# Performance work log

Measured on AMD Instinct MI355X. Metric: run time of the kernel, lower is better.

The kernel has to match this reference:

```python
import jax, jax.numpy as jnp
import numpy as np
from itertools import permutations as _permutations

N_ORB = 64
N_ALPHA = 5
N_BETA = 5
TEMP = 1.0
PERMS5 = jnp.asarray(np.array(list(_permutations(range(5))), dtype=np.int32))  # (120, 5)


def setup_inputs() -> dict:
    key = jax.random.key(0)
    ks = jax.random.split(key, 16)
    B = 8192
    s = 0.02
    inp = {
        "uniform_alpha": jax.random.uniform(ks[0], (B, N_ORB), dtype=jnp.float32),
        "uniform_beta": jax.random.uniform(ks[1], (B, N_ORB), dtype=jnp.float32),
        # learnable params
        "alpha_logits": jax.random.normal(ks[2], (N_ORB,), dtype=jnp.float32) * s,
        # alpha_to_beta: Linear(n_orb,128) -> SiLU -> Linear(128,64)
        "W1": jax.random.normal(ks[3], (N_ORB, 128), dtype=jnp.float32) * s,
        "b1": jnp.zeros((128,), jnp.float32),
        "W2": jax.random.normal(ks[4], (128, 64), dtype=jnp.float32) * s,
        "b2": jnp.zeros((64,), jnp.float32),
        # beta_conditioned_scorer: Linear(n_orb+64,256)->SiLU->Linear(256,256)->SiLU->Linear(256,n_orb)
        "V1": jax.random.normal(ks[5], (N_ORB + 64, 256), dtype=jnp.float32) * s,
        "c1": jnp.zeros((256,), jnp.float32),
        "V2": jax.random.normal(ks[6], (256, 256), dtype=jnp.float32) * s,
        "c2": jnp.zeros((256,), jnp.float32),
        "V3": jax.random.normal(ks[7], (256, N_ORB), dtype=jnp.float32) * s,
        "c3": jnp.zeros((N_ORB,), jnp.float32),
    }
    return inp


def _gumbel_topk(logits, uniform, k):
    """Straight-through Gumbel top-k mask. logits, uniform: (B, n)."""
    g = -jnp.log(-jnp.log(jnp.maximum(uniform, 1e-10)))
    perturbed = (logits + g) / TEMP
    _, top_idx = jax.lax.top_k(perturbed, k)                      # (B, k)
    B = logits.shape[0]
    one_hot = jnp.zeros_like(logits).at[jnp.arange(B)[:, None], top_idx].set(1.0)
    soft = jax.nn.softmax(perturbed, axis=-1)
    return one_hot - jax.lax.stop_gradient(soft) + soft


def _exact_pl_log_prob(logits, selection, k, perms):
    """log P(unordered top-k set) under Plackett-Luce, exact over k! orderings.

    logits: (B, n); selection: (B, n) soft/hard mask; perms: (P, k) static.
    """
    B, n = logits.shape
    P = perms.shape[0]
    _, sel_idx = jax.lax.top_k(selection, k)
    sel_idx = jnp.sort(sel_idx, axis=-1)                          # (B, k)
    perm_idx = sel_idx[:, perms]                                  # (B, P, k)
    lg = logits[:, None, :]                                       # (B, 1, n)
    remaining = jnp.ones((B, P, n), dtype=bool)
    lp = jnp.zeros((B, P), logits.dtype)
    bi = jnp.arange(B)[:, None]
    pi = jnp.arange(P)[None, :]
    for step in range(k):  # k is small and static (5)
        masked = jnp.where(remaining, lg, -jnp.inf)
        logp = jax.nn.log_softmax(masked, axis=-1)                # (B, P, n)
        idx = perm_idx[:, :, step]                                # (B, P)
        lp = lp + jnp.take_along_axis(logp, idx[..., None], axis=-1)[..., 0]
        remaining = remaining.at[bi, pi, idx].set(False)
    return jax.scipy.special.logsumexp(lp, axis=-1)              # (B,)


def reference(uniform_alpha, uniform_beta, alpha_logits, W1, b1, W2, b2,
              V1, c1, V2, c2, V3, c3):
    B = uniform_alpha.shape[0]
    a_logits = jnp.broadcast_to(alpha_logits[None, :], (B, N_ORB))
    alpha_config = _gumbel_topk(a_logits, uniform_alpha, N_ALPHA)

    # alpha_to_beta MLP
    h = jax.nn.silu(alpha_config @ W1 + b1)
    alpha_context = h @ W2 + b2                                   # (B, 64)

    beta_input = jnp.concatenate([jnp.zeros((B, N_ORB), a_logits.dtype), alpha_context], axis=-1)
    z = jax.nn.silu(beta_input @ V1 + c1)
    z = jax.nn.silu(z @ V2 + c2)
    beta_logits = z @ V3 + c3                                     # (B, n_orb)

    beta_config = _gumbel_topk(beta_logits, uniform_beta, N_BETA)
    configs = jnp.concatenate([alpha_config, beta_config], axis=-1)

    lp_a = _exact_pl_log_prob(a_logits, alpha_config, N_ALPHA, PERMS5)
    lp_b = _exact_pl_log_prob(beta_logits, beta_config, N_BETA, PERMS5)
    log_probs = lp_a + lp_b
    return configs, log_probs
```

## Files before the change

### kernel.cpp

```cpp
#include <hip/hip_runtime.h>
#include <math.h>

#define NTH 1024
#define KP 264
#define SPB 16
#define OFF_W2 0
#define OFF_V1 16384
#define OFF_V2 49152
#define OFF_V3 180224
#define WS_USHORTS 212992
#define MFMA16 __builtin_amdgcn_mfma_f32_16x16x32_bf16

typedef __attribute__((ext_vector_type(8))) short s16x8;
typedef __attribute__((ext_vector_type(8))) unsigned short u16x8;
typedef __attribute__((ext_vector_type(4))) float f32x4;

__device__ __forceinline__ float waveSum(float v) {
#pragma unroll
  for (int off = 32; off; off >>= 1) v += __shfl_xor(v, off, 64);
  return v;
}

__device__ __forceinline__ float siluf(float x) { return x / (1.0f + __expf(-x)); }

__device__ __forceinline__ unsigned short bround(float x) {
  unsigned u = __float_as_uint(x);
  return (unsigned short)((u + 0x7FFFu + ((u >> 16) & 1u)) >> 16);
}

__device__ __forceinline__ void bsplit(float x, unsigned short& h, unsigned short& l) {
  unsigned u = __float_as_uint(x);
  unsigned hb = (u + 0x7FFFu + ((u >> 16) & 1u)) >> 16;
  float hf = __uint_as_float(hb << 16);
  float lf = x - hf;
  unsigned ul = __float_as_uint(lf);
  unsigned lb = (ul + 0x7FFFu + ((ul >> 16) & 1u)) >> 16;
  h = (unsigned short)hb; l = (unsigned short)lb;
}

__device__ __forceinline__ float permSum(const float se0, const float se1,
                                         const float se2, const float se3,
                                         const float se4, float Z, int lane) {
  float psum = 0.0f;
#pragma unroll
  for (int pp = 0; pp < 2; ++pp) {
    int p = lane + pp * 64;
    if (p < 120) {
      int rem = p;
      unsigned avail = 0x43210u;
      float c = 0.0f;
      float prod = Z;
#pragma unroll
      for (int j = 0; j < 4; ++j) {
        const int fct = (j == 0) ? 24 : (j == 1) ? 6 : (j == 2) ? 2 : 1;
        int q = rem / fct; rem -= q * fct;
        int sh = q * 4;
        int dg = (avail >> sh) & 0xF;
        avail = (avail & ((1u << sh) - 1u)) | ((avail >> (sh + 4)) << sh);
        float ev = (dg == 0) ? se0 : (dg == 1) ? se1 : (dg == 2) ? se2
                 : (dg == 3) ? se3 : se4;
        c += ev;
        prod *= (Z - c);
      }
      psum += __builtin_amdgcn_rcpf(prod);
    }
  }
  return psum;
}

__device__ __forceinline__ float selectAndPL(float lv, float ev, float Z,
                                             float g,
                                             float* __restrict__ gout,
                                             int lane,
                                             float* __restrict__ sValsRow,
                                             float* __restrict__ sSelERow,
                                             int* __restrict__ selIdxRow) {
  float v = lv + g;
  sValsRow[lane] = v;
  int rank = 0;
#pragma unroll
  for (int j = 0; j < 16; ++j) {
    float4 w = *(const float4*)&sValsRow[j * 4];
    int base = j * 4;
    rank += (w.x > v || (w.x == v && base + 0 < lane)) ? 1 : 0;
    rank += (w.y > v || (w.y == v && base + 1 < lane)) ? 1 : 0;
    rank += (w.z > v || (w.z == v && base + 2 < lane)) ? 1 : 0;
    rank += (w.w > v || (w.w == v && base + 3 < lane)) ? 1 : 0;
  }
  bool sel = rank < 5;
  gout[lane] = sel ? 1.0f : 0.0f;
  if (sel) {
    sSelERow[rank] = ev;
    sSelERow[8 + rank] = lv;
    if (selIdxRow) selIdxRow[rank] = lane;
  }
  float se0 = sSelERow[0], se1 = sSelERow[1], se2 = sSelERow[2],
        se3 = sSelERow[3], se4 = sSelERow[4];
  float sl = sSelERow[8] + sSelERow[9] + sSelERow[10] + sSelERow[11]
           + sSelERow[12];
  float S = waveSum(permSum(se0, se1, se2, se3, se4, Z, lane));
  return sl + __logf(S);
}

__global__ __launch_bounds__(256)
void pcf_prep(const float* __restrict__ W2, const float* __restrict__ V1,
              const float* __restrict__ V2, const float* __restrict__ V3,
              unsigned short* __restrict__ ws)
{
  int tid = blockIdx.x * 256 + threadIdx.x;
  const float* src; int N, Ks, dstoff, r;
  if (tid < 1024)       { src = W2;            N = 64;  Ks = 4; dstoff = OFF_W2; r = tid; }
  else if (tid < 3072)  { src = V1 + 64 * 256; N = 256; Ks = 2; dstoff = OFF_V1; r = tid - 1024; }
  else if (tid < 11264) { src = V2;            N = 256; Ks = 8; dstoff = OFF_V2; r = tid - 3072; }
  else                  { src = V3;            N = 64;  Ks = 8; dstoff = OFF_V3; r = tid - 11264; }
  int lane = r & 63, ts = r >> 6;
  int ks = ts % Ks, ct = ts / Ks;
  int n = ct * 16 + (lane & 15);
  int k0 = ks * 32 + (lane >> 4) * 8;
  u16x8 hv, lv;
#pragma unroll
  for (int j = 0; j < 8; ++j) {
    float x = src[(size_t)(k0 + j) * N + n];
    unsigned short h, l;
    bsplit(x, h, l);
    hv[j] = h; lv[j] = l;
  }
  unsigned short* dst = ws + dstoff + (size_t)ts * 1024 + lane * 8;
  *(u16x8*)dst = hv;
  *(u16x8*)(dst + 512) = lv;
}

__global__ __launch_bounds__(NTH, 8)
void pcf_mfma(const float* __restrict__ ua, const float* __restrict__ ub,
              const float* __restrict__ alog, const float* __restrict__ W1,
              const float* __restrict__ b1, const float* __restrict__ b2,
              const float* __restrict__ c1, const float* __restrict__ c2,
              const float* __restrict__ c3,
              const unsigned short* __restrict__ wt, float* __restrict__ out)
{
  __shared__ unsigned short sAhi[16 * KP];
  __shared__ unsigned short sBhi[16 * KP];
  __shared__ float sBL[SPB * 64];
  __shared__ float sVals[SPB * 64];
  __shared__ float sSelE[SPB * 16];
  __shared__ int   sSelA[SPB * 5];
  __shared__ float sLpA[SPB];

  const int t    = threadIdx.x;
  const int lane = t & 63;
  const int wv   = t >> 6;
  const int ln15 = lane & 15;
  const int quad = lane >> 4;
  const int bbase = blockIdx.x * SPB;

  float gb;
  {
    int b = bbase + wv;
    float u = ub[(size_t)b * 64 + lane];
    gb = -logf(-logf(fmaxf(u, 1e-10f)));
  }

  {
    float la = alog[lane];
    float ea = __expf(la);
    float Za = waveSum(ea);
    int b = bbase + wv;
    float u = ua[(size_t)b * 64 + lane];
    float ga = -logf(-logf(fmaxf(u, 1e-10f)));
    float lp = selectAndPL(la, ea, Za, ga, out + (size_t)b * 128, lane,
                           &sVals[wv * 64], &sSelE[wv * 16], &sSelA[wv * 5]);
    if (lane == 0) sLpA[wv] = lp;
  }
  __syncthreads();

  {
    int s = wv;
    int j = lane * 2;
    const int rows[5] = { sSelA[s * 5 + 0], sSelA[s * 5 + 1], sSelA[s * 5 + 2],
                          sSelA[s * 5 + 3], sSelA[s * 5 + 4] };
    float2 a = *(const float2*)(b1 + j);
#pragma unroll
    for (int r = 0; r < 5; ++r) {
      float2 w = *(const float2*)(W1 + (size_t)rows[r] * 128 + j);
      a.x += w.x; a.y += w.y;
    }
    unsigned h0 = bround(siluf(a.x));
    unsigned h1 = bround(siluf(a.y));
    *(unsigned*)&sAhi[s * KP + j] = h0 | (h1 << 16);
  }
  __syncthreads();

  if (wv < 4) {
    f32x4 acc = {0.f, 0.f, 0.f, 0.f};
#pragma unroll
    for (int ks = 0; ks < 4; ++ks) {
      int ko = ks * 32 + quad * 8;
      s16x8 ah = *(const s16x8*)&sAhi[ln15 * KP + ko];
      const unsigned short* tsb = wt + OFF_W2 + (size_t)(wv * 4 + ks) * 1024;
      s16x8 bh = ((const s16x8*)tsb)[lane];
      s16x8 bl = ((const s16x8*)(tsb + 512))[lane];
      acc = MFMA16(ah, bh, acc, 0, 0, 0);
      acc = MFMA16(ah, bl, acc, 0, 0, 0);
    }
    int col = wv * 16 + ln15;
    float bias = b2[col];
#pragma unroll
    for (int r = 0; r < 4; ++r)
      sBhi[(quad * 4 + r) * KP + col] = bround(acc[r] + bias);
  }
  __syncthreads();

  {
    f32x4 acc = {0.f, 0.f, 0.f, 0.f};
#pragma unroll
    for (int ks = 0; ks < 2; ++ks) {
      int ko = ks * 32 + quad * 8;
      s16x8 ah = *(const s16x8*)&sBhi[ln15 * KP + ko];
      const unsigned short* tsb = wt + OFF_V1 + (size_t)(wv * 2 + ks) * 1024;
      s16x8 bh = ((const s16x8*)tsb)[lane];
      s16x8 bl = ((const s16x8*)(tsb + 512))[lane];
      acc = MFMA16(ah, bh, acc, 0, 0, 0);
      acc = MFMA16(ah, bl, acc, 0, 0, 0);
    }
    int col = wv * 16 + ln15;
    float bias = c1[col];
#pragma unroll
    for (int r = 0; r < 4; ++r)
      sAhi[(quad * 4 + r) * KP + col] = bround(siluf(acc[r] + bias));
  }
  __syncthreads();

  {
    f32x4 acc = {0.f, 0.f, 0.f, 0.f};
#pragma unroll 4
    for (int ks = 0; ks < 8; ++ks) {
      int ko = ks * 32 + quad * 8;
      s16x8 ah = *(const s16x8*)&sAhi[ln15 * KP + ko];
      const unsigned short* tsb = wt + OFF_V2 + (size_t)(wv * 8 + ks) * 1024;
      s16x8 bh = ((const s16x8*)tsb)[lane];
      s16x8 bl = ((const s16x8*)(tsb + 512))[lane];
      acc = MFMA16(ah, bh, acc, 0, 0, 0);
      acc = MFMA16(ah, bl, acc, 0, 0, 0);
    }
    int col = wv * 16 + ln15;
    float bias = c2[col];
#pragma unroll
    for (int r = 0; r < 4; ++r)
      sBhi[(quad * 4 + r) * KP + col] = bround(siluf(acc[r] + bias));
  }
  __syncthreads();

  if (wv < 4) {
    f32x4 acc = {0.f, 0.f, 0.f, 0.f};
#pragma unroll
    for (int ks = 0; ks < 8; ++ks) {
      int ko = ks * 32 + quad * 8;
      s16x8 ah = *(const s16x8*)&sBhi[ln15 * KP + ko];
      const unsigned short* tsb = wt + OFF_V3 + (size_t)(wv * 8 + ks) * 1024;
      s16x8 bh = ((const s16x8*)tsb)[lane];
      s16x8 bl = ((const s16x8*)(tsb + 512))[lane];
      acc = MFMA16(ah, bh, acc, 0, 0, 0);
      acc = MFMA16(ah, bl, acc, 0, 0, 0);
    }
    int col = wv * 16 + ln15;
    float bias = c3[col];
#pragma unroll
    for (int r = 0; r < 4; ++r)
      sBL[(quad * 4 + r) * 64 + col] = acc[r] + bias;
  }
  __syncthreads();

  {
    int b = bbase + wv;
    float blv = sBL[wv * 64 + lane];
    float eb = __expf(blv);
    float Zb = waveSum(eb);
    float lp = selectAndPL(blv, eb, Zb, gb,
                           out + (size_t)b * 128 + 64, lane,
                           &sVals[wv * 64], &sSelE[wv * 16], nullptr);
    if (lane == 0)
      out[(size_t)8192 * 128 + b] = sLpA[wv] + lp;
  }
}

#define SPB4 4
__global__ __launch_bounds__(256, 8)
void pcf_small(const float* __restrict__ ua, const float* __restrict__ ub,
               const float* __restrict__ alog, const float* __restrict__ W1,
               const float* __restrict__ b1, const float* __restrict__ W2,
               const float* __restrict__ b2, const float* __restrict__ V1,
               const float* __restrict__ c1, const float* __restrict__ V2,
               const float* __restrict__ c2, const float* __restrict__ V3,
               const float* __restrict__ c3, float* __restrict__ out)
{
  __shared__ float sA[SPB4 * 256];
  __shared__ float sB[SPB4 * 256];
  __shared__ float sP[4 * 256];
  __shared__ float sVals[4 * 64];
  __shared__ float sSelE[4 * 16];
  __shared__ int   sSelA[SPB4 * 5];
  __shared__ float sLpA[SPB4];

  const int t    = threadIdx.x;
  const int lane = t & 63;
  const int wv   = t >> 6;
  const int bbase = blockIdx.x * SPB4;

  float* sValsRow = &sVals[wv * 64];
  float* sSelERow = &sSelE[wv * 16];

  {
    float la = alog[lane];
    float ea = __expf(la);
    float Za = waveSum(ea);
    int b = bbase + wv;
    float u = ua[(size_t)b * 64 + lane];
    float g = -logf(-logf(fmaxf(u, 1e-10f)));
    float lp = selectAndPL(la, ea, Za, g, out + (size_t)b * 128, lane,
                           sValsRow, sSelERow, &sSelA[wv * 5]);
    if (lane == 0) sLpA[wv] = lp;
  }
  __syncthreads();
  {
    int s = wv;
    int i0 = sSelA[s * 5 + 0], i1 = sSelA[s * 5 + 1], i2 = sSelA[s * 5 + 2];
    int i3 = sSelA[s * 5 + 3], i4 = sSelA[s * 5 + 4];
#pragma unroll
    for (int jh = 0; jh < 2; ++jh) {
      int j = lane + jh * 64;
      float acc = b1[j] + W1[i0 * 128 + j] + W1[i1 * 128 + j]
                + W1[i2 * 128 + j] + W1[i3 * 128 + j] + W1[i4 * 128 + j];
      sA[s * 128 + j] = siluf(acc);
    }
  }
  __syncthreads();
  {
    float acc[SPB4] = {};
    const int kb = 32 * wv;
#pragma unroll 2
    for (int m = 0; m < 8; ++m) {
      int k0 = kb + 4 * m;
      float w0 = W2[(k0 + 0) * 64 + lane];
      float w1 = W2[(k0 + 1) * 64 + lane];
      float w2 = W2[(k0 + 2) * 64 + lane];
      float w3 = W2[(k0 + 3) * 64 + lane];
#pragma unroll
      for (int s = 0; s < SPB4; ++s) {
        float4 x = *(float4*)&sA[s * 128 + k0];
        acc[s] += x.x * w0 + x.y * w1 + x.z * w2 + x.w * w3;
      }
    }
#pragma unroll
    for (int s = 0; s < SPB4; ++s) sP[wv * 256 + s * 64 + lane] = acc[s];
  }
  __syncthreads();
  {
    int o = t;
    float v = b2[o & 63] + sP[o] + sP[256 + o] + sP[512 + o] + sP[768 + o];
    sB[o] = v;
  }
  __syncthreads();
  {
    const int c = 64 * wv + lane;
    float acc[SPB4];
    float cb = c1[c];
#pragma unroll
    for (int s = 0; s < SPB4; ++s) acc[s] = cb;
    const float* wp = V1 + (size_t)64 * 256 + c;
#pragma unroll 4
    for (int m = 0; m < 16; ++m) {
      int k0 = 4 * m;
      float w0 = wp[(k0 + 0) * 256];
      float w1 = wp[(k0 + 1) * 256];
      float w2 = wp[(k0 + 2) * 256];
      float w3 = wp[(k0 + 3) * 256];
#pragma unroll
      for (int s = 0; s < SPB4; ++s) {
        float4 x = *(float4*)&sB[s * 64 + k0];
        acc[s] += x.x * w0 + x.y * w1 + x.z * w2 + x.w * w3;
      }
    }
#pragma unroll
    for (int s = 0; s < SPB4; ++s) sA[s * 256 + c] = siluf(acc[s]);
  }
  __syncthreads();
  {
    const int c = 64 * wv + lane;
    float acc[SPB4];
    float cb = c2[c];
#pragma unroll
    for (int s = 0; s < SPB4; ++s) acc[s] = cb;
    const float* wp = V2 + c;
#pragma unroll 4
    for (int m = 0; m < 64; ++m) {
      int k0 = 4 * m;
      float w0 = wp[(size_t)(k0 + 0) * 256];
      float w1 = wp[(size_t)(k0 + 1) * 256];
      float w2 = wp[(size_t)(k0 + 2) * 256];
      float w3 = wp[(size_t)(k0 + 3) * 256];
#pragma unroll
      for (int s = 0; s < SPB4; ++s) {
        float4 x = *(float4*)&sA[s * 256 + k0];
        acc[s] += x.x * w0 + x.y * w1 + x.z * w2 + x.w * w3;
      }
    }
#pragma unroll
    for (int s = 0; s < SPB4; ++s) sB[s * 256 + c] = siluf(acc[s]);
  }
  __syncthreads();
  {
    float acc[SPB4] = {};
    const int kb = 64 * wv;
#pragma unroll 4
    for (int m = 0; m < 16; ++m) {
      int k0 = kb + 4 * m;
      float w0 = V3[(k0 + 0) * 64 + lane];
      float w1 = V3[(k0 + 1) * 64 + lane];
      float w2 = V3[(k0 + 2) * 64 + lane];
      float w3 = V3[(k0 + 3) * 64 + lane];
#pragma unroll
      for (int s = 0; s < SPB4; ++s) {
        float4 x = *(float4*)&sB[s * 256 + k0];
        acc[s] += x.x * w0 + x.y * w1 + x.z * w2 + x.w * w3;
      }
    }
#pragma unroll
    for (int s = 0; s < SPB4; ++s) sP[wv * 256 + s * 64 + lane] = acc[s];
  }
  __syncthreads();
  {
    int b = bbase + wv;
    float blv = c3[lane] + sP[wv * 64 + lane] + sP[256 + wv * 64 + lane]
              + sP[512 + wv * 64 + lane] + sP[768 + wv * 64 + lane];
    float eb = __expf(blv);
    float Zb = waveSum(eb);
    float u = ub[(size_t)b * 64 + lane];
    float g = -logf(-logf(fmaxf(u, 1e-10f)));
    float lp = selectAndPL(blv, eb, Zb, g, out + (size_t)b * 128 + 64, lane,
                           sValsRow, sSelERow, nullptr);
    if (lane == 0)
      out[(size_t)8192 * 128 + b] = sLpA[wv] + lp;
  }
}

extern "C" void kernel_launch(void* const* d_in, const int* in_sizes, int n_in,
                              void* d_out, int out_size, void* d_ws, size_t ws_size,
                              hipStream_t stream) {
  const float* ua   = (const float*)d_in[0];
  const float* ub   = (const float*)d_in[1];
  const float* alog = (const float*)d_in[2];
  const float* W1   = (const float*)d_in[3];
  const float* b1   = (const float*)d_in[4];
  const float* W2   = (const float*)d_in[5];
  const float* b2   = (const float*)d_in[6];
  const float* V1   = (const float*)d_in[7];
  const float* c1   = (const float*)d_in[8];
  const float* V2   = (const float*)d_in[9];
  const float* c2   = (const float*)d_in[10];
  const float* V3   = (const float*)d_in[11];
  const float* c3   = (const float*)d_in[12];
  float* out = (float*)d_out;

  if (ws_size >= (size_t)WS_USHORTS * 2) {
    unsigned short* wt = (unsigned short*)d_ws;
    pcf_prep<<<dim3(52), dim3(256), 0, stream>>>(W2, V1, V2, V3, wt);
    pcf_mfma<<<dim3(8192 / SPB), dim3(NTH), 0, stream>>>(
        ua, ub, alog, W1, b1, b2, c1, c2, c3, wt, out);
  } else {
    pcf_small<<<dim3(8192 / SPB4), dim3(256), 0, stream>>>(
        ua, ub, alog, W1, b1, W2, b2, V1, c1, V2, c2, V3, c3, out);
  }
}
```

Measured before the change: 106.3 us.

## Drop weight prep kernel and split fp32 weights into bf16 fragments inside the MFMA kernel

Removes the separate prep kernel that pre-split weights into hi/lo bf16 tiles in workspace. Each wave now loads fp32 weight columns directly (strided 8-row gathers) and does the bf16 split in registers before every MFMA. This removes one kernel launch and the workspace round trip. In exchange, 512 blocks redo the split and issue uncoalesced strided loads instead of one vector load per fragment. The small-workspace fallback kernel is also deleted and some unroll factors are lowered.

```diff
diff --git a/kernel.cpp b/kernel.cpp
--- a/kernel.cpp
+++ b/kernel.cpp
@@ -4,15 +4,9 @@
 #define NTH 1024
 #define KP 264
 #define SPB 16
-#define OFF_W2 0
-#define OFF_V1 16384
-#define OFF_V2 49152
-#define OFF_V3 180224
-#define WS_USHORTS 212992
 #define MFMA16 __builtin_amdgcn_mfma_f32_16x16x32_bf16
 
 typedef __attribute__((ext_vector_type(8))) short s16x8;
-typedef __attribute__((ext_vector_type(8))) unsigned short u16x8;
 typedef __attribute__((ext_vector_type(4))) float f32x4;
 
 __device__ __forceinline__ float waveSum(float v) {
@@ -36,6 +30,21 @@
   unsigned ul = __float_as_uint(lf);
   unsigned lb = (ul + 0x7FFFu + ((ul >> 16) & 1u)) >> 16;
   h = (unsigned short)hb; l = (unsigned short)lb;
+}
+
+__device__ __forceinline__ void loadFrag(const float* __restrict__ src,
+                                         const int N, int k0, int n,
+                                         s16x8& hv, s16x8& lv) {
+  const float* p = src + (size_t)k0 * N + n;
+  float x[8];
+#pragma unroll
+  for (int j = 0; j < 8; ++j) x[j] = p[(size_t)j * N];
+#pragma unroll
+  for (int j = 0; j < 8; ++j) {
+    unsigned short h, l;
+    bsplit(x[j], h, l);
+    hv[j] = (short)h; lv[j] = (short)l;
+  }
 }
 
 __device__ __forceinline__ float permSum(const float se0, const float se1,
@@ -102,41 +111,14 @@
   return sl + __logf(S);
 }
 
-__global__ __launch_bounds__(256)
-void pcf_prep(const float* __restrict__ W2, const float* __restrict__ V1,
-              const float* __restrict__ V2, const float* __restrict__ V3,
-              unsigned short* __restrict__ ws)
-{
-  int tid = blockIdx.x * 256 + threadIdx.x;
-  const float* src; int N, Ks, dstoff, r;
-  if (tid < 1024)       { src = W2;            N = 64;  Ks = 4; dstoff = OFF_W2; r = tid; }
-  else if (tid < 3072)  { src = V1 + 64 * 256; N = 256; Ks = 2; dstoff = OFF_V1; r = tid - 1024; }
-  else if (tid < 11264) { src = V2;            N = 256; Ks = 8; dstoff = OFF_V2; r = tid - 3072; }
-  else                  { src = V3;            N = 64;  Ks = 8; dstoff = OFF_V3; r = tid - 11264; }
-  int lane = r & 63, ts = r >> 6;
-  int ks = ts % Ks, ct = ts / Ks;
-  int n = ct * 16 + (lane & 15);
-  int k0 = ks * 32 + (lane >> 4) * 8;
-  u16x8 hv, lv;
-#pragma unroll
-  for (int j = 0; j < 8; ++j) {
-    float x = src[(size_t)(k0 + j) * N + n];
-    unsigned short h, l;
-    bsplit(x, h, l);
-    hv[j] = h; lv[j] = l;
-  }
-  unsigned short* dst = ws + dstoff + (size_t)ts * 1024 + lane * 8;
-  *(u16x8*)dst = hv;
-  *(u16x8*)(dst + 512) = lv;
-}
-
 __global__ __launch_bounds__(NTH, 8)
 void pcf_mfma(const float* __restrict__ ua, const float* __restrict__ ub,
               const float* __restrict__ alog, const float* __restrict__ W1,
-              const float* __restrict__ b1, const float* __restrict__ b2,
-              const float* __restrict__ c1, const float* __restrict__ c2,
-              const float* __restrict__ c3,
-              const unsigned short* __restrict__ wt, float* __restrict__ out)
+              const float* __restrict__ b1, const float* __restrict__ W2,
+              const float* __restrict__ b2, const float* __restrict__ V1,
+              const float* __restrict__ c1, const float* __restrict__ V2,
+              const float* __restrict__ c2, const float* __restrict__ V3,
+              const float* __restrict__ c3, float* __restrict__ out)
 {
   __shared__ unsigned short sAhi[16 * KP];
   __shared__ unsigned short sBhi[16 * KP];
@@ -152,6 +134,8 @@
   const int ln15 = lane & 15;
   const int quad = lane >> 4;
   const int bbase = blockIdx.x * SPB;
+  const int fk0  = quad * 8;
+  const int fcol = wv * 16 + ln15;
 
   float gb;
   {
@@ -192,81 +176,74 @@
 
   if (wv < 4) {
     f32x4 acc = {0.f, 0.f, 0.f, 0.f};
-#pragma unroll
+#pragma unroll 2
     for (int ks = 0; ks < 4; ++ks) {
-      int ko = ks * 32 + quad * 8;
+      int ko = ks * 32 + fk0;
       s16x8 ah = *(const s16x8*)&sAhi[ln15 * KP + ko];
-      const unsigned short* tsb = wt + OFF_W2 + (size_t)(wv * 4 + ks) * 1024;
-      s16x8 bh = ((const s16x8*)tsb)[lane];
-      s16x8 bl = ((const s16x8*)(tsb + 512))[lane];
-      acc = MFMA16(ah, bh, acc, 0, 0, 0);
-      acc = MFMA16(ah, bl, acc, 0, 0, 0);
-    }
-    int col = wv * 16 + ln15;
-    float bias = b2[col];
-#pragma unroll
-    for (int r = 0; r < 4; ++r)
-      sBhi[(quad * 4 + r) * KP + col] = bround(acc[r] + bias);
-  }
-  __syncthreads();
-
-  {
+      s16x8 bh, bl;
+      loadFrag(W2, 64, ko, fcol, bh, bl);
+      acc = MFMA16(ah, bh, acc, 0, 0, 0);
+      acc = MFMA16(ah, bl, acc, 0, 0, 0);
+    }
+    float bias = b2[fcol];
+#pragma unroll
+    for (int r = 0; r < 4; ++r)
+      sBhi[(quad * 4 + r) * KP + fcol] = bround(acc[r] + bias);
+  }
+  __syncthreads();
+
+  {
+    const float* V1f = V1 + (size_t)64 * 256;
     f32x4 acc = {0.f, 0.f, 0.f, 0.f};
 #pragma unroll
     for (int ks = 0; ks < 2; ++ks) {
-      int ko = ks * 32 + quad * 8;
+      int ko = ks * 32 + fk0;
       s16x8 ah = *(const s16x8*)&sBhi[ln15 * KP + ko];
-      const unsigned short* tsb = wt + OFF_V1 + (size_t)(wv * 2 + ks) * 1024;
-      s16x8 bh = ((const s16x8*)tsb)[lane];
-      s16x8 bl = ((const s16x8*)(tsb + 512))[lane];
-      acc = MFMA16(ah, bh, acc, 0, 0, 0);
-      acc = MFMA16(ah, bl, acc, 0, 0, 0);
-    }
-    int col = wv * 16 + ln15;
-    float bias = c1[col];
-#pragma unroll
-    for (int r = 0; r < 4; ++r)
-      sAhi[(quad * 4 + r) * KP + col] = bround(siluf(acc[r] + bias));
-  }
-  __syncthreads();
-
-  {
-    f32x4 acc = {0.f, 0.f, 0.f, 0.f};
-#pragma unroll 4
+      s16x8 bh, bl;
+      loadFrag(V1f, 256, ko, fcol, bh, bl);
+      acc = MFMA16(ah, bh, acc, 0, 0, 0);
+      acc = MFMA16(ah, bl, acc, 0, 0, 0);
+    }
+    float bias = c1[fcol];
+#pragma unroll
+    for (int r = 0; r < 4; ++r)
+      sAhi[(quad * 4 + r) * KP + fcol] = bround(siluf(acc[r] + bias));
+  }
+  __syncthreads();
+
+  {
+    f32x4 acc = {0.f, 0.f, 0.f, 0.f};
+#pragma unroll 2
     for (int ks = 0; ks < 8; ++ks) {
-      int ko = ks * 32 + quad * 8;
+      int ko = ks * 32 + fk0;
       s16x8 ah = *(const s16x8*)&sAhi[ln15 * KP + ko];
-      const unsigned short* tsb = wt + OFF_V2 + (size_t)(wv * 8 + ks) * 1024;
-      s16x8 bh = ((const s16x8*)tsb)[lane];
-      s16x8 bl = ((const s16x8*)(tsb + 512))[lane];
-      acc = MFMA16(ah, bh, acc, 0, 0, 0);
-      acc = MFMA16(ah, bl, acc, 0, 0, 0);
-    }
-    int col = wv * 16 + ln15;
-    float bias = c2[col];
-#pragma unroll
-    for (int r = 0; r < 4; ++r)
-      sBhi[(quad * 4 + r) * KP + col] = bround(siluf(acc[r] + bias));
+      s16x8 bh, bl;
+      loadFrag(V2, 256, ko, fcol, bh, bl);
+      acc = MFMA16(ah, bh, acc, 0, 0, 0);
+      acc = MFMA16(ah, bl, acc, 0, 0, 0);
+    }
+    float bias = c2[fcol];
+#pragma unroll
+    for (int r = 0; r < 4; ++r)
+      sBhi[(quad * 4 + r) * KP + fcol] = bround(siluf(acc[r] + bias));
   }
   __syncthreads();
 
   if (wv < 4) {
     f32x4 acc = {0.f, 0.f, 0.f, 0.f};
-#pragma unroll
+#pragma unroll 2
     for (int ks = 0; ks < 8; ++ks) {
-      int ko = ks * 32 + quad * 8;
+      int ko = ks * 32 + fk0;
       s16x8 ah = *(const s16x8*)&sBhi[ln15 * KP + ko];
-      const unsigned short* tsb = wt + OFF_V3 + (size_t)(wv * 8 + ks) * 1024;
-      s16x8 bh = ((const s16x8*)tsb)[lane];
-      s16x8 bl = ((const s16x8*)(tsb + 512))[lane];
-      acc = MFMA16(ah, bh, acc, 0, 0, 0);
-      acc = MFMA16(ah, bl, acc, 0, 0, 0);
-    }
-    int col = wv * 16 + ln15;
-    float bias = c3[col];
-#pragma unroll
-    for (int r = 0; r < 4; ++r)
-      sBL[(quad * 4 + r) * 64 + col] = acc[r] + bias;
+      s16x8 bh, bl;
+      loadFrag(V3, 64, ko, fcol, bh, bl);
+      acc = MFMA16(ah, bh, acc, 0, 0, 0);
+      acc = MFMA16(ah, bl, acc, 0, 0, 0);
+    }
+    float bias = c3[fcol];
+#pragma unroll
+    for (int r = 0; r < 4; ++r)
+      sBL[(quad * 4 + r) * 64 + fcol] = acc[r] + bias;
   }
   __syncthreads();
 
@@ -278,166 +255,6 @@
     float lp = selectAndPL(blv, eb, Zb, gb,
                            out + (size_t)b * 128 + 64, lane,
                            &sVals[wv * 64], &sSelE[wv * 16], nullptr);
-    if (lane == 0)
-      out[(size_t)8192 * 128 + b] = sLpA[wv] + lp;
-  }
-}
-
-#define SPB4 4
-__global__ __launch_bounds__(256, 8)
-void pcf_small(const float* __restrict__ ua, const float* __restrict__ ub,
-               const float* __restrict__ alog, const float* __restrict__ W1,
-               const float* __restrict__ b1, const float* __restrict__ W2,
-               const float* __restrict__ b2, const float* __restrict__ V1,
-               const float* __restrict__ c1, const float* __restrict__ V2,
-               const float* __restrict__ c2, const float* __restrict__ V3,
-               const float* __restrict__ c3, float* __restrict__ out)
-{
-  __shared__ float sA[SPB4 * 256];
-  __shared__ float sB[SPB4 * 256];
-  __shared__ float sP[4 * 256];
-  __shared__ float sVals[4 * 64];
-  __shared__ float sSelE[4 * 16];
-  __shared__ int   sSelA[SPB4 * 5];
-  __shared__ float sLpA[SPB4];
-
-  const int t    = threadIdx.x;
-  const int lane = t & 63;
-  const int wv   = t >> 6;
-  const int bbase = blockIdx.x * SPB4;
-
-  float* sValsRow = &sVals[wv * 64];
-  float* sSelERow = &sSelE[wv * 16];
-
-  {
-    float la = alog[lane];
-    float ea = __expf(la);
-    float Za = waveSum(ea);
-    int b = bbase + wv;
-    float u = ua[(size_t)b * 64 + lane];
-    float g = -logf(-logf(fmaxf(u, 1e-10f)));
-    float lp = selectAndPL(la, ea, Za, g, out + (size_t)b * 128, lane,
-                           sValsRow, sSelERow, &sSelA[wv * 5]);
-    if (lane == 0) sLpA[wv] = lp;
-  }
-  __syncthreads();
-  {
-    int s = wv;
-    int i0 = sSelA[s * 5 + 0], i1 = sSelA[s * 5 + 1], i2 = sSelA[s * 5 + 2];
-    int i3 = sSelA[s * 5 + 3], i4 = sSelA[s * 5 + 4];
-#pragma unroll
-    for (int jh = 0; jh < 2; ++jh) {
-      int j = lane + jh * 64;
-      float acc = b1[j] + W1[i0 * 128 + j] + W1[i1 * 128 + j]
-                + W1[i2 * 128 + j] + W1[i3 * 128 + j] + W1[i4 * 128 + j];
-      sA[s * 128 + j] = siluf(acc);
-    }
-  }
-  __syncthreads();
-  {
-    float acc[SPB4] = {};
-    const int kb = 32 * wv;
-#pragma unroll 2
-    for (int m = 0; m < 8; ++m) {
-      int k0 = kb + 4 * m;
-      float w0 = W2[(k0 + 0) * 64 + lane];
-      float w1 = W2[(k0 + 1) * 64 + lane];
-      float w2 = W2[(k0 + 2) * 64 + lane];
-      float w3 = W2[(k0 + 3) * 64 + lane];
-#pragma unroll
-      for (int s = 0; s < SPB4; ++s) {
-        float4 x = *(float4*)&sA[s * 128 + k0];
-        acc[s] += x.x * w0 + x.y * w1 + x.z * w2 + x.w * w3;
-      }
-    }
-#pragma unroll
-    for (int s = 0; s < SPB4; ++s) sP[wv * 256 + s * 64 + lane] = acc[s];
-  }
-  __syncthreads();
-  {
-    int o = t;
-    float v = b2[o & 63] + sP[o] + sP[256 + o] + sP[512 + o] + sP[768 + o];
-    sB[o] = v;
-  }
-  __syncthreads();
-  {
-    const int c = 64 * wv + lane;
-    float acc[SPB4];
-    float cb = c1[c];
-#pragma unroll
-    for (int s = 0; s < SPB4; ++s) acc[s] = cb;
-    const float* wp = V1 + (size_t)64 * 256 + c;
-#pragma unroll 4
-    for (int m = 0; m < 16; ++m) {
-      int k0 = 4 * m;
-      float w0 = wp[(k0 + 0) * 256];
-      float w1 = wp[(k0 + 1) * 256];
-      float w2 = wp[(k0 + 2) * 256];
-      float w3 = wp[(k0 + 3) * 256];
-#pragma unroll
-      for (int s = 0; s < SPB4; ++s) {
-        float4 x = *(float4*)&sB[s * 64 + k0];
-        acc[s] += x.x * w0 + x.y * w1 + x.z * w2 + x.w * w3;
-      }
-    }
-#pragma unroll
-    for (int s = 0; s < SPB4; ++s) sA[s * 256 + c] = siluf(acc[s]);
-  }
-  __syncthreads();
-  {
-    const int c = 64 * wv + lane;
-    float acc[SPB4];
-    float cb = c2[c];
-#pragma unroll
-    for (int s = 0; s < SPB4; ++s) acc[s] = cb;
-    const float* wp = V2 + c;
-#pragma unroll 4
-    for (int m = 0; m < 64; ++m) {
-      int k0 = 4 * m;
-      float w0 = wp[(size_t)(k0 + 0) * 256];
-      float w1 = wp[(size_t)(k0 + 1) * 256];
-      float w2 = wp[(size_t)(k0 + 2) * 256];
-      float w3 = wp[(size_t)(k0 + 3) * 256];
-#pragma unroll
-      for (int s = 0; s < SPB4; ++s) {
-        float4 x = *(float4*)&sA[s * 256 + k0];
-        acc[s] += x.x * w0 + x.y * w1 + x.z * w2 + x.w * w3;
-      }
-    }
-#pragma unroll
-    for (int s = 0; s < SPB4; ++s) sB[s * 256 + c] = siluf(acc[s]);
-  }
-  __syncthreads();
-  {
-    float acc[SPB4] = {};
-    const int kb = 64 * wv;
-#pragma unroll 4
-    for (int m = 0; m < 16; ++m) {
-      int k0 = kb + 4 * m;
-      float w0 = V3[(k0 + 0) * 64 + lane];
-      float w1 = V3[(k0 + 1) * 64 + lane];
-      float w2 = V3[(k0 + 2) * 64 + lane];
-      float w3 = V3[(k0 + 3) * 64 + lane];
-#pragma unroll
-      for (int s = 0; s < SPB4; ++s) {
-        float4 x = *(float4*)&sB[s * 256 + k0];
-        acc[s] += x.x * w0 + x.y * w1 + x.z * w2 + x.w * w3;
-      }
-    }
-#pragma unroll
-    for (int s = 0; s < SPB4; ++s) sP[wv * 256 + s * 64 + lane] = acc[s];
-  }
-  __syncthreads();
-  {
-    int b = bbase + wv;
-    float blv = c3[lane] + sP[wv * 64 + lane] + sP[256 + wv * 64 + lane]
-              + sP[512 + wv * 64 + lane] + sP[768 + wv * 64 + lane];
-    float eb = __expf(blv);
-    float Zb = waveSum(eb);
-    float u = ub[(size_t)b * 64 + lane];
-    float g = -logf(-logf(fmaxf(u, 1e-10f)));
-    float lp = selectAndPL(blv, eb, Zb, g, out + (size_t)b * 128 + 64, lane,
-                           sValsRow, sSelERow, nullptr);
     if (lane == 0)
       out[(size_t)8192 * 128 + b] = sLpA[wv] + lp;
   }
@@ -461,13 +278,7 @@
   const float* c3   = (const float*)d_in[12];
   float* out = (float*)d_out;
 
-  if (ws_size >= (size_t)WS_USHORTS * 2) {
-    unsigned short* wt = (unsigned short*)d_ws;
-    pcf_prep<<<dim3(52), dim3(256), 0, stream>>>(W2, V1, V2, V3, wt);
-    pcf_mfma<<<dim3(8192 / SPB), dim3(NTH), 0, stream>>>(
-        ua, ub, alog, W1, b1, b2, c1, c2, c3, wt, out);
-  } else {
-    pcf_small<<<dim3(8192 / SPB4), dim3(256), 0, stream>>>(
-        ua, ub, alog, W1, b1, W2, b2, V1, c1, V2, c2, V3, c3, out);
-  }
-}
+  (void)d_ws; (void)ws_size;
+  pcf_mfma<<<dim3(8192 / SPB), dim3(NTH), 0, stream>>>(
+      ua, ub, alog, W1, b1, W2, b2, V1, c1, V2, c2, V3, c3, out);
+}
```

After: 113.5 us. +6.7%, slower.
